# Kernel tuning notes

Hardware: AMD Instinct MI355X
Metric: run time of the kernel (lower is better)

The kernel has to match this reference:

```python
import jax, jax.numpy as jnp
import numpy as np

B, L, NF = 8, 4096, 256
NEG = jnp.float32(-1e30)
EPS = 1e-4  # scn BatchNormReLU default eps


def setup_inputs() -> dict:
    key = jax.random.key(0)
    ks = jax.random.split(key, 5)
    x = jax.random.normal(ks[0], (B, L, NF), dtype=jnp.float32)
    # ragged segment lengths -> padded mask
    lens = np.random.default_rng(0).integers(L // 2, L + 1, size=B)
    mask = jnp.asarray(np.arange(L)[None, :] < lens[:, None])  # [B, L] bool
    s = 1.0 / np.sqrt(NF)
    Wq = jax.random.normal(ks[1], (NF, NF), dtype=jnp.float32) * s
    Wk = jax.random.normal(ks[2], (NF, NF), dtype=jnp.float32) * s
    Wv = jax.random.normal(ks[3], (NF, NF), dtype=jnp.float32) * s
    Wt = jax.random.normal(ks[4], (NF, NF), dtype=jnp.float32) * s
    gamma = jnp.ones((NF,), dtype=jnp.float32)
    beta = jnp.zeros((NF,), dtype=jnp.float32)
    return {"x": x, "mask": mask, "Wq": Wq, "Wk": Wk, "Wv": Wv,
            "Wt": Wt, "gamma": gamma, "beta": beta}


def reference(x, mask, Wq, Wk, Wv, Wt, gamma, beta):
    m = mask.astype(x.dtype)[:, :, None]          # [B, L, 1] validity
    q = jnp.einsum('bld,de->ble', x, Wq)
    k = jnp.einsum('bld,de->ble', x, Wk)
    v = jnp.einsum('bld,de->ble', x, Wv)
    # per-segment full attention (unscaled QK^T, as in the original module)
    scores = jnp.einsum('bld,bmd->blm', q, k)     # [B, L, L]
    scores = jnp.where(mask[:, None, :], scores, NEG)
    p = jax.nn.softmax(scores, axis=-1)
    attn = jnp.einsum('blm,bmd->bld', p, v)
    t = jnp.einsum('bld,de->ble', attn, Wt)
    # BatchNormReLU over all valid points (masked batch stats per channel)
    n = jnp.sum(m)
    mean = jnp.sum(t * m, axis=(0, 1)) / n
    var = jnp.sum(jnp.square(t - mean) * m, axis=(0, 1)) / n
    y = gamma * (t - mean) * jax.lax.rsqrt(var + EPS) + beta
    y = jax.nn.relu(y)
    out = (x + y) * m                             # residual, zero padding
    return out
```

## Files before the change

### kernel.cpp

```cpp
#include <hip/hip_runtime.h>
#include <cmath>

typedef _Float16 f16;
typedef f16 f16x8 __attribute__((ext_vector_type(8)));
typedef f16 f16x4 __attribute__((ext_vector_type(4)));
typedef float f32x4 __attribute__((ext_vector_type(4)));

#define Ln 4096
#define Dn 256
#define NEGV (-1e30f)

#define B_QH   0ul
#define B_KH   (16ul << 20)
#define B_VT   (32ul << 20)
#define B_OP   (48ul << 20)
#define B_ML   (80ul << 20)
#define B_ATH  0ul
#define B_T    (16ul << 20)
#define B_LENS (81ul << 20)
#define B_SUMS (B_LENS + 128)
#define B_WQT  (B_LENS + 4096)
#define B_WKT  (B_WQT + (128ul<<10))
#define B_WVT  (B_WKT + (128ul<<10))
#define B_WTT  (B_WVT + (128ul<<10))

__device__ __forceinline__ void async_ld16(f16* lds, const f16* g) {
  __builtin_amdgcn_global_load_lds((const __attribute__((address_space(1))) unsigned int*)g,
                                   (__attribute__((address_space(3))) unsigned int*)lds, 16, 0, 0);
}

__global__ __launch_bounds__(256) void k_init(const int* __restrict__ mask, int* __restrict__ lens,
                                              float* __restrict__ sums) {
  const int b = blockIdx.x, tid = threadIdx.x;
  if (b == 0) { sums[tid] = 0.f; sums[256 + tid] = 0.f; }
  int cnt = 0;
  for (int l = tid; l < Ln; l += 256) cnt += (mask[b * Ln + l] != 0) ? 1 : 0;
  __shared__ int red[256];
  red[tid] = cnt;
  __syncthreads();
  for (int s = 128; s > 0; s >>= 1) {
    if (tid < s) red[tid] += red[tid + s];
    __syncthreads();
  }
  if (tid == 0) lens[b] = red[0];
}

__global__ __launch_bounds__(256) void k_cast_w(const float* __restrict__ W0, const float* __restrict__ W1,
                                                const float* __restrict__ W2, const float* __restrict__ W3,
                                                f16* __restrict__ T0, f16* __restrict__ T1,
                                                f16* __restrict__ T2, f16* __restrict__ T3) {
  const float* Ws[4] = {W0, W1, W2, W3};
  f16* Ts[4] = {T0, T1, T2, T3};
  const float* W = Ws[blockIdx.x];
  f16* T = Ts[blockIdx.x];
  const int k0 = blockIdx.y * 64, n0 = blockIdx.z * 64;
  const int tid = threadIdx.x;
  __shared__ float ld[64][65];
#pragma unroll
  for (int i = 0; i < 16; ++i) {
    int flat = i * 256 + tid;
    int r = flat >> 6, c = flat & 63;
    ld[r][c] = W[(size_t)(k0 + r) * Dn + n0 + c];
  }
  __syncthreads();
#pragma unroll
  for (int i = 0; i < 16; ++i) {
    int flat = i * 256 + tid;
    int r = flat >> 6, c = flat & 63;
    T[(size_t)(n0 + r) * Dn + k0 + c] = (f16)ld[c][r];
  }
}

__global__ __launch_bounds__(256) void k_qkv(const float* __restrict__ x, const f16* __restrict__ WqT,
                                             const f16* __restrict__ WkT, const f16* __restrict__ WvT,
                                             f16* __restrict__ Qh, f16* __restrict__ Kh,
                                             f16* __restrict__ Vt) {
  __shared__ f16 sA[64 * 256];
  __shared__ f16 vts[256 * 72];
  const int tid = threadIdx.x;
  const int lane = tid & 63;
  const int ln15 = lane & 15;
  const int quad = lane >> 4;
  const int wave = tid >> 6;
  const int wr = wave >> 1;
  const int wn = wave & 1;
  const size_t row0 = (size_t)blockIdx.x * 64;

  {
    const float* src = x + row0 * Dn;
#pragma unroll
    for (int i = 0; i < 8; ++i) {
      int flat = i * 256 + tid;
      int r = flat >> 5, p = flat & 31, g = p ^ (r & 7);
      float4 lo = *(const float4*)&src[r * Dn + g * 8];
      float4 hi = *(const float4*)&src[r * Dn + g * 8 + 4];
      f16x8 h = {(f16)lo.x, (f16)lo.y, (f16)lo.z, (f16)lo.w,
                 (f16)hi.x, (f16)hi.y, (f16)hi.z, (f16)hi.w};
      *(f16x8*)&sA[flat * 8] = h;
    }
  }
  __syncthreads();

  f16x8 af[2][8];
#pragma unroll
  for (int rg = 0; rg < 2; ++rg) {
    int r = wr * 32 + rg * 16 + ln15;
    int sw = r & 7;
#pragma unroll
    for (int c = 0; c < 8; ++c)
      af[rg][c] = *(const f16x8*)&sA[r * 256 + (((c * 4 + quad) ^ sw) << 3)];
  }

  const f16* Bm[3] = {WqT, WkT, WvT};
  for (int m = 0; m < 3; ++m) {
    const f16* B = Bm[m];
    f32x4 acc0[8], acc1[8];
#pragma unroll
    for (int nt = 0; nt < 8; ++nt) {
#pragma unroll
      for (int i = 0; i < 4; ++i) { acc0[nt][i] = 0.f; acc1[nt][i] = 0.f; }
    }
#pragma unroll
    for (int c = 0; c < 8; ++c) {
#pragma unroll
      for (int nt = 0; nt < 8; ++nt) {
        f16x8 bf = *(const f16x8*)&B[(size_t)(wn * 128 + nt * 16 + ln15) * 256 + c * 32 + quad * 8];
        acc0[nt] = __builtin_amdgcn_mfma_f32_16x16x32_f16(af[0][c], bf, acc0[nt], 0, 0, 0);
        acc1[nt] = __builtin_amdgcn_mfma_f32_16x16x32_f16(af[1][c], bf, acc1[nt], 0, 0, 0);
      }
    }
    if (m < 2) {
      f16* dst = (m == 0) ? Qh : Kh;
#pragma unroll
      for (int nt = 0; nt < 8; ++nt) {
        int col = wn * 128 + nt * 16 + ln15;
#pragma unroll
        for (int i = 0; i < 4; ++i) {
          dst[(row0 + wr * 32 + quad * 4 + i) * (size_t)Dn + col] = (f16)acc0[nt][i];
          dst[(row0 + wr * 32 + 16 + quad * 4 + i) * (size_t)Dn + col] = (f16)acc1[nt][i];
        }
      }
    } else {
#pragma unroll
      for (int nt = 0; nt < 8; ++nt) {
        int ch = wn * 128 + nt * 16 + ln15;
#pragma unroll
        for (int i = 0; i < 4; ++i) {
          vts[ch * 72 + wr * 32 + quad * 4 + i] = (f16)acc0[nt][i];
          vts[ch * 72 + wr * 32 + 16 + quad * 4 + i] = (f16)acc1[nt][i];
        }
      }
      __syncthreads();
      const int b = (int)(row0 >> 12);
      const int l0 = (int)(row0 & 4095);
      f16* vdst = Vt + (size_t)b * Dn * Ln + (size_t)tid * Ln + l0;
#pragma unroll
      for (int j = 0; j < 8; ++j)
        *(f16x8*)(vdst + 8 * j) = *(const f16x8*)&vts[tid * 72 + 8 * j];
    }
  }
}

__global__ __launch_bounds__(256, 3) void k_flash(const f16* __restrict__ Qh, const f16* __restrict__ Kh,
                                                  const f16* __restrict__ Vt, const int* __restrict__ lens,
                                                  f16* __restrict__ Op, float2* __restrict__ Ml) {
  const int b = blockIdx.z;
  const int s = blockIdx.y;
  const int len = lens[b];
  const int i0 = blockIdx.x * 64;
  if (i0 >= len) return;
  const int tid = threadIdx.x;
  const int lane = tid & 63;
  const int ln15 = lane & 15;
  const int quad = lane >> 4;
  const int w = tid >> 6;

  __shared__ f16 sK[32 * 256];
  __shared__ f16 sV[256 * 32];
  __shared__ f16 sP[4][16 * 40];

  const f16* Qb = Qh + (size_t)b * Ln * Dn;
  const f16* Kb = Kh + (size_t)b * Ln * Dn;
  const f16* Vb = Vt + (size_t)b * Dn * Ln;

  const int T = (len + 31) >> 5;
  const int h = T >> 1;
  const int t0 = s ? h : 0;
  const int t1 = s ? T : h;

  f16x8 qf[8];
  {
    const f16* qrow = Qb + (size_t)(i0 + w * 16 + ln15) * Dn + quad * 8;
#pragma unroll
    for (int c = 0; c < 8; ++c) qf[c] = *(const f16x8*)(qrow + c * 32);
  }

  f32x4 oAcc[16];
#pragma unroll
  for (int nf = 0; nf < 16; ++nf) { oAcc[nf][0] = 0.f; oAcc[nf][1] = 0.f; oAcc[nf][2] = 0.f; oAcc[nf][3] = 0.f; }
  float m_i[4], l_i[4];
#pragma unroll
  for (int i = 0; i < 4; ++i) { m_i[i] = -INFINITY; l_i[i] = 0.f; }

  for (int t = t0; t < t1; ++t) {
    const int j0 = t << 5;
    __syncthreads();
    {
      const f16* ksrc = Kb + (size_t)j0 * Dn;
#pragma unroll
      for (int i = 0; i < 4; ++i) {
        int flat = i * 256 + tid;
        int r = flat >> 5, p = flat & 31, g = p ^ (r & 7);
        async_ld16(&sK[(i * 256 + (tid & 192)) * 8], ksrc + r * Dn + g * 8);
      }
#pragma unroll
      for (int i = 0; i < 4; ++i) {
        int flat = i * 256 + tid;
        int r = flat >> 2, p = flat & 3, g = p ^ (r & 3);
        async_ld16(&sV[(i * 256 + (tid & 192)) * 8], Vb + (size_t)r * Ln + j0 + g * 8);
      }
    }
    __syncthreads();

    f32x4 sa0, sa1;
    sa0[0] = sa0[1] = sa0[2] = sa0[3] = 0.f;
    sa1[0] = sa1[1] = sa1[2] = sa1[3] = 0.f;
    const int swz = ln15 & 7;
#pragma unroll
    for (int c = 0; c < 8; ++c) {
      int gk = (((c * 4 + quad) ^ swz) << 3);
      f16x8 b0 = *(const f16x8*)&sK[ln15 * 256 + gk];
      f16x8 b1 = *(const f16x8*)&sK[(16 + ln15) * 256 + gk];
      sa0 = __builtin_amdgcn_mfma_f32_16x16x32_f16(qf[c], b0, sa0, 0, 0, 0);
      sa1 = __builtin_amdgcn_mfma_f32_16x16x32_f16(qf[c], b1, sa1, 0, 0, 0);
    }

    const bool iv0 = (j0 + ln15) >= len;
    const bool iv1 = (j0 + 16 + ln15) >= len;
    float alpha[4];
    bool need = false;
#pragma unroll
    for (int i = 0; i < 4; ++i) {
      float a0 = iv0 ? NEGV : sa0[i];
      float a1 = iv1 ? NEGV : sa1[i];
      float rm = fmaxf(a0, a1);
      rm = fmaxf(rm, __shfl_xor(rm, 1));
      rm = fmaxf(rm, __shfl_xor(rm, 2));
      rm = fmaxf(rm, __shfl_xor(rm, 4));
      rm = fmaxf(rm, __shfl_xor(rm, 8));
      float mo = m_i[i];
      float mn = fmaxf(mo, rm);
      float al = __expf(mo - mn);
      float p0 = __expf(a0 - mn);
      float p1 = __expf(a1 - mn);
      float rs = p0 + p1;
      rs += __shfl_xor(rs, 1);
      rs += __shfl_xor(rs, 2);
      rs += __shfl_xor(rs, 4);
      rs += __shfl_xor(rs, 8);
      l_i[i] = l_i[i] * al + rs;
      m_i[i] = mn;
      alpha[i] = al;
      need |= (al < 1.0f);
      sP[w][(quad * 4 + i) * 40 + ln15] = (f16)p0;
      sP[w][(quad * 4 + i) * 40 + 16 + ln15] = (f16)p1;
    }
    if (__any(need ? 1 : 0)) {
#pragma unroll
      for (int nf = 0; nf < 16; ++nf)
#pragma unroll
        for (int i = 0; i < 4; ++i) oAcc[nf][i] *= alpha[i];
    }

    f16x8 pa = *(const f16x8*)&sP[w][ln15 * 40 + quad * 8];
#pragma unroll
    for (int nf = 0; nf < 16; ++nf) {
      int ch = nf * 16 + ln15;
      f16x8 vb = *(const f16x8*)&sV[ch * 32 + ((quad ^ (ch & 3)) << 3)];
      oAcc[nf] = __builtin_amdgcn_mfma_f32_16x16x32_f16(pa, vb, oAcc[nf], 0, 0, 0);
    }
  }

  f16* Ob = Op + ((size_t)s * 8 + b) * Ln * Dn;
  float2* Mb = Ml + ((size_t)s * 8 + b) * Ln;
#pragma unroll
  for (int i = 0; i < 4; ++i) {
    int row = i0 + w * 16 + quad * 4 + i;
    if (row < len) {
      float inv = 1.f / l_i[i];
#pragma unroll
      for (int nf = 0; nf < 16; ++nf)
        Ob[(size_t)row * Dn + nf * 16 + ln15] = (f16)(oAcc[nf][i] * inv);
      if (ln15 == 0) Mb[row] = make_float2(m_i[i], l_i[i]);
    }
  }
}

__global__ __launch_bounds__(256) void k_combine(const f16* __restrict__ Op, const float2* __restrict__ Ml,
                                                 const int* __restrict__ lens, f16* __restrict__ ath) {
  const size_t idx = (size_t)blockIdx.x * 256 + threadIdx.x;
  const size_t rowg = idx >> 6;
  const int b = (int)(rowg >> 12);
  const int row = (int)(rowg & 4095);
  if (row >= lens[b]) return;
  const size_t SS = (size_t)8 * Ln * Dn;
  float2 ml0 = Ml[(size_t)b * Ln + row];
  float2 ml1 = Ml[(size_t)8 * Ln + (size_t)b * Ln + row];
  float ms = fmaxf(ml0.x, ml1.x);
  float w0 = __expf(ml0.x - ms) * ml0.y;
  float w1 = __expf(ml1.x - ms) * ml1.y;
  float inv = 1.f / (w0 + w1);
  w0 *= inv; w1 *= inv;
  const size_t off = rowg * Dn + (idx & 63) * 4;
  f16x4 p0 = *(const f16x4*)&Op[off];
  f16x4 p1 = *(const f16x4*)&Op[SS + off];
  f16x4 o;
#pragma unroll
  for (int j = 0; j < 4; ++j) o[j] = (f16)(w0 * (float)p0[j] + w1 * (float)p1[j]);
  *(f16x4*)&ath[off] = o;
}

__global__ __launch_bounds__(256) void k_t(const f16* __restrict__ ah, const f16* __restrict__ WtT,
                                           const int* __restrict__ mask, float* __restrict__ t,
                                           float* __restrict__ sums) {
  __shared__ f16 sA[64 * 256];
  __shared__ float sSum[256];
  __shared__ float sSq[256];
  const int tid = threadIdx.x;
  const int lane = tid & 63;
  const int ln15 = lane & 15;
  const int quad = lane >> 4;
  const int wave = tid >> 6;
  const int wr = wave >> 1;
  const int wn = wave & 1;
  const size_t row0 = (size_t)blockIdx.x * 64;
  sSum[tid] = 0.f;
  sSq[tid] = 0.f;
  {
    const f16* src = ah + row0 * Dn;
#pragma unroll
    for (int i = 0; i < 8; ++i) {
      int flat = i * 256 + tid;
      int r = flat >> 5, p = flat & 31, g = p ^ (r & 7);
      async_ld16(&sA[(i * 256 + (tid & 192)) * 8], src + r * 256 + g * 8);
    }
  }
  __syncthreads();
  f16x8 af[2][8];
#pragma unroll
  for (int rg = 0; rg < 2; ++rg) {
    int r = wr * 32 + rg * 16 + ln15;
    int sw = r & 7;
#pragma unroll
    for (int c = 0; c < 8; ++c)
      af[rg][c] = *(const f16x8*)&sA[r * 256 + (((c * 4 + quad) ^ sw) << 3)];
  }
  f32x4 acc0[8], acc1[8];
#pragma unroll
  for (int nt = 0; nt < 8; ++nt) {
#pragma unroll
    for (int i = 0; i < 4; ++i) { acc0[nt][i] = 0.f; acc1[nt][i] = 0.f; }
  }
#pragma unroll
  for (int c = 0; c < 8; ++c) {
#pragma unroll
    for (int nt = 0; nt < 8; ++nt) {
      f16x8 bf = *(const f16x8*)&WtT[(size_t)(wn * 128 + nt * 16 + ln15) * 256 + c * 32 + quad * 8];
      acc0[nt] = __builtin_amdgcn_mfma_f32_16x16x32_f16(af[0][c], bf, acc0[nt], 0, 0, 0);
      acc1[nt] = __builtin_amdgcn_mfma_f32_16x16x32_f16(af[1][c], bf, acc1[nt], 0, 0, 0);
    }
  }
  float msk0[4], msk1[4];
#pragma unroll
  for (int i = 0; i < 4; ++i) {
    size_t r = row0 + wr * 32 + quad * 4 + i;
    msk0[i] = (mask[r] != 0) ? 1.f : 0.f;
    msk1[i] = (mask[r + 16] != 0) ? 1.f : 0.f;
  }
#pragma unroll
  for (int nt = 0; nt < 8; ++nt) {
    int col = wn * 128 + nt * 16 + ln15;
    float ps = 0.f, pq = 0.f;
#pragma unroll
    for (int i = 0; i < 4; ++i) {
      float v0 = acc0[nt][i], v1 = acc1[nt][i];
      t[(row0 + wr * 32 + quad * 4 + i) * (size_t)Dn + col] = v0;
      t[(row0 + wr * 32 + 16 + quad * 4 + i) * (size_t)Dn + col] = v1;
      ps += v0 * msk0[i] + v1 * msk1[i];
      pq += v0 * v0 * msk0[i] + v1 * v1 * msk1[i];
    }
    ps += __shfl_xor(ps, 16); ps += __shfl_xor(ps, 32);
    pq += __shfl_xor(pq, 16); pq += __shfl_xor(pq, 32);
    if (quad == 0) {
      atomicAdd(&sSum[col], ps);
      atomicAdd(&sSq[col], pq);
    }
  }
  __syncthreads();
  atomicAdd(&sums[tid], sSum[tid]);
  atomicAdd(&sums[256 + tid], sSq[tid]);
}

__device__ __forceinline__ float bn_relu(float tv, int ch, float fn, const float* sums,
                                         const float* gamma, const float* beta) {
  float mean = sums[ch] / fn;
  float var = sums[256 + ch] / fn - mean * mean;
  float y = gamma[ch] * (tv - mean) * rsqrtf(var + 1e-4f) + beta[ch];
  return y > 0.f ? y : 0.f;
}

__global__ __launch_bounds__(256) void k_final(const float* __restrict__ x, const int* __restrict__ mask,
                                               const float* __restrict__ t, const float* __restrict__ gamma,
                                               const float* __restrict__ beta, const float* __restrict__ sums,
                                               const int* __restrict__ lens, float* __restrict__ out) {
  const size_t idx = (size_t)blockIdx.x * 256 + threadIdx.x;
  const size_t row = idx >> 6;
  const int c = (int)(idx & 63) * 4;
  float4 o;
  if (mask[row] == 0) {
    o = make_float4(0.f, 0.f, 0.f, 0.f);
  } else {
    int n = 0;
#pragma unroll
    for (int i = 0; i < 8; ++i) n += lens[i];
    const float fn = (float)n;
    float4 tv = *(const float4*)&t[row * Dn + c];
    float4 xv = *(const float4*)&x[row * Dn + c];
    o.x = xv.x + bn_relu(tv.x, c + 0, fn, sums, gamma, beta);
    o.y = xv.y + bn_relu(tv.y, c + 1, fn, sums, gamma, beta);
    o.z = xv.z + bn_relu(tv.z, c + 2, fn, sums, gamma, beta);
    o.w = xv.w + bn_relu(tv.w, c + 3, fn, sums, gamma, beta);
  }
  *(float4*)&out[idx * 4] = o;
}

extern "C" void kernel_launch(void* const* d_in, const int* in_sizes, int n_in,
                              void* d_out, int out_size, void* d_ws, size_t ws_size,
                              hipStream_t stream) {
  const float* x = (const float*)d_in[0];
  const int* mask = (const int*)d_in[1];
  const float* Wq = (const float*)d_in[2];
  const float* Wk = (const float*)d_in[3];
  const float* Wv = (const float*)d_in[4];
  const float* Wt = (const float*)d_in[5];
  const float* gamma = (const float*)d_in[6];
  const float* beta = (const float*)d_in[7];
  float* out = (float*)d_out;
  char* wsb = (char*)d_ws;

  f16* Qh = (f16*)(wsb + B_QH);
  f16* Kh = (f16*)(wsb + B_KH);
  f16* Vt = (f16*)(wsb + B_VT);
  f16* Op = (f16*)(wsb + B_OP);
  float2* Ml = (float2*)(wsb + B_ML);
  f16* ath = (f16*)(wsb + B_ATH);
  float* t = (float*)(wsb + B_T);
  int* lens = (int*)(wsb + B_LENS);
  float* sums = (float*)(wsb + B_SUMS);
  f16* WqT = (f16*)(wsb + B_WQT);
  f16* WkT = (f16*)(wsb + B_WKT);
  f16* WvT = (f16*)(wsb + B_WVT);
  f16* WtT = (f16*)(wsb + B_WTT);

  k_init<<<8, 256, 0, stream>>>(mask, lens, sums);
  k_cast_w<<<dim3(4, 4, 4), 256, 0, stream>>>(Wq, Wk, Wv, Wt, WqT, WkT, WvT, WtT);
  k_qkv<<<512, 256, 0, stream>>>(x, WqT, WkT, WvT, Qh, Kh, Vt);
  k_flash<<<dim3(64, 2, 8), 256, 0, stream>>>(Qh, Kh, Vt, lens, Op, Ml);
  k_combine<<<8192, 256, 0, stream>>>(Op, Ml, lens, ath);
  k_t<<<512, 256, 0, stream>>>(ath, WtT, mask, t, sums);
  k_final<<<8192, 256, 0, stream>>>(x, mask, t, gamma, beta, sums, lens, out);
}
```

Baseline: 463.2 us.

## Split flash attention three ways, fold combine into projection, MFMA row sums

The key range in the flash kernel is now split into three parts instead of two, giving more blocks to spread across the GPU. The separate combine kernel is removed: the output-projection kernel now reads the three partial outputs and their max/sum statistics, merges them with softmax weights while filling LDS, and then does the GEMM. The per-row softmax denominator is accumulated with an MFMA against a ones vector instead of shuffle reductions. In exchange it writes and reads a third partial output buffer, repeats the Q loads for each split, and replaces async LDS loads in the projection kernel with synchronous loads plus arithmetic.

After: 395.0 us. 1.17x faster.

```diff
diff --git a/kernel.cpp b/kernel.cpp
--- a/kernel.cpp
+++ b/kernel.cpp
@@ -14,10 +14,9 @@
 #define B_KH   (16ul << 20)
 #define B_VT   (32ul << 20)
 #define B_OP   (48ul << 20)
-#define B_ML   (80ul << 20)
-#define B_ATH  0ul
+#define B_ML   (96ul << 20)
 #define B_T    (16ul << 20)
-#define B_LENS (81ul << 20)
+#define B_LENS ((97ul << 20))
 #define B_SUMS (B_LENS + 128)
 #define B_WQT  (B_LENS + 4096)
 #define B_WKT  (B_WQT + (128ul<<10))
@@ -184,9 +183,8 @@
   const f16* Vb = Vt + (size_t)b * Dn * Ln;
 
   const int T = (len + 31) >> 5;
-  const int h = T >> 1;
-  const int t0 = s ? h : 0;
-  const int t1 = s ? T : h;
+  const int t0 = (s * T) / 3;
+  const int t1 = ((s + 1) * T) / 3;
 
   f16x8 qf[8];
   {
@@ -198,9 +196,13 @@
   f32x4 oAcc[16];
 #pragma unroll
   for (int nf = 0; nf < 16; ++nf) { oAcc[nf][0] = 0.f; oAcc[nf][1] = 0.f; oAcc[nf][2] = 0.f; oAcc[nf][3] = 0.f; }
-  float m_i[4], l_i[4];
-#pragma unroll
-  for (int i = 0; i < 4; ++i) { m_i[i] = -INFINITY; l_i[i] = 0.f; }
+  f32x4 lAcc;
+  lAcc[0] = lAcc[1] = lAcc[2] = lAcc[3] = 0.f;
+  float m_i[4];
+#pragma unroll
+  for (int i = 0; i < 4; ++i) m_i[i] = -INFINITY;
+  const f16x8 onesf = {(f16)1.f, (f16)1.f, (f16)1.f, (f16)1.f,
+                       (f16)1.f, (f16)1.f, (f16)1.f, (f16)1.f};
 
   for (int t = t0; t < t1; ++t) {
     const int j0 = t << 5;
@@ -253,12 +255,6 @@
       float al = __expf(mo - mn);
       float p0 = __expf(a0 - mn);
       float p1 = __expf(a1 - mn);
-      float rs = p0 + p1;
-      rs += __shfl_xor(rs, 1);
-      rs += __shfl_xor(rs, 2);
-      rs += __shfl_xor(rs, 4);
-      rs += __shfl_xor(rs, 8);
-      l_i[i] = l_i[i] * al + rs;
       m_i[i] = mn;
       alpha[i] = al;
       need |= (al < 1.0f);
@@ -270,9 +266,12 @@
       for (int nf = 0; nf < 16; ++nf)
 #pragma unroll
         for (int i = 0; i < 4; ++i) oAcc[nf][i] *= alpha[i];
+#pragma unroll
+      for (int i = 0; i < 4; ++i) lAcc[i] *= alpha[i];
     }
 
     f16x8 pa = *(const f16x8*)&sP[w][ln15 * 40 + quad * 8];
+    lAcc = __builtin_amdgcn_mfma_f32_16x16x32_f16(pa, onesf, lAcc, 0, 0, 0);
 #pragma unroll
     for (int nf = 0; nf < 16; ++nf) {
       int ch = nf * 16 + ln15;
@@ -281,49 +280,27 @@
     }
   }
 
-  f16* Ob = Op + ((size_t)s * 8 + b) * Ln * Dn;
+  f16* Ob = Op + (size_t)s * (8ul * Ln * Dn) + (size_t)b * Ln * Dn;
   float2* Mb = Ml + ((size_t)s * 8 + b) * Ln;
 #pragma unroll
   for (int i = 0; i < 4; ++i) {
     int row = i0 + w * 16 + quad * 4 + i;
     if (row < len) {
-      float inv = 1.f / l_i[i];
+      float inv = 1.f / lAcc[i];
 #pragma unroll
       for (int nf = 0; nf < 16; ++nf)
         Ob[(size_t)row * Dn + nf * 16 + ln15] = (f16)(oAcc[nf][i] * inv);
-      if (ln15 == 0) Mb[row] = make_float2(m_i[i], l_i[i]);
-    }
-  }
-}
-
-__global__ __launch_bounds__(256) void k_combine(const f16* __restrict__ Op, const float2* __restrict__ Ml,
-                                                 const int* __restrict__ lens, f16* __restrict__ ath) {
-  const size_t idx = (size_t)blockIdx.x * 256 + threadIdx.x;
-  const size_t rowg = idx >> 6;
-  const int b = (int)(rowg >> 12);
-  const int row = (int)(rowg & 4095);
-  if (row >= lens[b]) return;
-  const size_t SS = (size_t)8 * Ln * Dn;
-  float2 ml0 = Ml[(size_t)b * Ln + row];
-  float2 ml1 = Ml[(size_t)8 * Ln + (size_t)b * Ln + row];
-  float ms = fmaxf(ml0.x, ml1.x);
-  float w0 = __expf(ml0.x - ms) * ml0.y;
-  float w1 = __expf(ml1.x - ms) * ml1.y;
-  float inv = 1.f / (w0 + w1);
-  w0 *= inv; w1 *= inv;
-  const size_t off = rowg * Dn + (idx & 63) * 4;
-  f16x4 p0 = *(const f16x4*)&Op[off];
-  f16x4 p1 = *(const f16x4*)&Op[SS + off];
-  f16x4 o;
-#pragma unroll
-  for (int j = 0; j < 4; ++j) o[j] = (f16)(w0 * (float)p0[j] + w1 * (float)p1[j]);
-  *(f16x4*)&ath[off] = o;
-}
-
-__global__ __launch_bounds__(256) void k_t(const f16* __restrict__ ah, const f16* __restrict__ WtT,
-                                           const int* __restrict__ mask, float* __restrict__ t,
+      if (ln15 == 0) Mb[row] = make_float2(m_i[i], lAcc[i]);
+    }
+  }
+}
+
+__global__ __launch_bounds__(256) void k_t(const f16* __restrict__ Op, const float2* __restrict__ Ml,
+                                           const f16* __restrict__ WtT, const int* __restrict__ mask,
+                                           const int* __restrict__ lens, float* __restrict__ t,
                                            float* __restrict__ sums) {
   __shared__ f16 sA[64 * 256];
+  __shared__ float sW[3][64];
   __shared__ float sSum[256];
   __shared__ float sSq[256];
   const int tid = threadIdx.x;
@@ -334,16 +311,42 @@
   const int wr = wave >> 1;
   const int wn = wave & 1;
   const size_t row0 = (size_t)blockIdx.x * 64;
+  const int b = (int)(row0 >> 12);
+  const int r0loc = (int)(row0 & 4095);
+  const size_t SS = 8ul * Ln * Dn;
   sSum[tid] = 0.f;
   sSq[tid] = 0.f;
-  {
-    const f16* src = ah + row0 * Dn;
-#pragma unroll
-    for (int i = 0; i < 8; ++i) {
-      int flat = i * 256 + tid;
-      int r = flat >> 5, p = flat & 31, g = p ^ (r & 7);
-      async_ld16(&sA[(i * 256 + (tid & 192)) * 8], src + r * 256 + g * 8);
-    }
+  if (tid < 64) {
+    int rl = r0loc + tid;
+    float w0 = 0.f, w1 = 0.f, w2 = 0.f;
+    if (rl < lens[b]) {
+      float2 m0 = Ml[(size_t)(0 * 8 + b) * Ln + rl];
+      float2 m1 = Ml[(size_t)(1 * 8 + b) * Ln + rl];
+      float2 m2 = Ml[(size_t)(2 * 8 + b) * Ln + rl];
+      float ms = fmaxf(m0.x, fmaxf(m1.x, m2.x));
+      w0 = __expf(m0.x - ms) * m0.y;
+      w1 = __expf(m1.x - ms) * m1.y;
+      w2 = __expf(m2.x - ms) * m2.y;
+      float inv = 1.f / (w0 + w1 + w2);
+      w0 *= inv; w1 *= inv; w2 *= inv;
+    }
+    sW[0][tid] = w0; sW[1][tid] = w1; sW[2][tid] = w2;
+  }
+  __syncthreads();
+#pragma unroll
+  for (int i = 0; i < 8; ++i) {
+    int flat = i * 256 + tid;
+    int r = flat >> 5, p = flat & 31, g = p ^ (r & 7);
+    size_t off = (row0 + r) * (size_t)Dn + g * 8;
+    f16x8 p0 = *(const f16x8*)&Op[off];
+    f16x8 p1 = *(const f16x8*)&Op[SS + off];
+    f16x8 p2 = *(const f16x8*)&Op[2 * SS + off];
+    float w0 = sW[0][r], w1 = sW[1][r], w2 = sW[2][r];
+    f16x8 h;
+#pragma unroll
+    for (int j = 0; j < 8; ++j)
+      h[j] = (f16)(w0 * (float)p0[j] + w1 * (float)p1[j] + w2 * (float)p2[j]);
+    *(f16x8*)&sA[flat * 8] = h;
   }
   __syncthreads();
   f16x8 af[2][8];
@@ -453,7 +456,6 @@
   f16* Vt = (f16*)(wsb + B_VT);
   f16* Op = (f16*)(wsb + B_OP);
   float2* Ml = (float2*)(wsb + B_ML);
-  f16* ath = (f16*)(wsb + B_ATH);
   float* t = (float*)(wsb + B_T);
   int* lens = (int*)(wsb + B_LENS);
   float* sums = (float*)(wsb + B_SUMS);
@@ -465,8 +467,7 @@
   k_init<<<8, 256, 0, stream>>>(mask, lens, sums);
   k_cast_w<<<dim3(4, 4, 4), 256, 0, stream>>>(Wq, Wk, Wv, Wt, WqT, WkT, WvT, WtT);
   k_qkv<<<512, 256, 0, stream>>>(x, WqT, WkT, WvT, Qh, Kh, Vt);
-  k_flash<<<dim3(64, 2, 8), 256, 0, stream>>>(Qh, Kh, Vt, lens, Op, Ml);
-  k_combine<<<8192, 256, 0, stream>>>(Op, Ml, lens, ath);
-  k_t<<<512, 256, 0, stream>>>(ath, WtT, mask, t, sums);
+  k_flash<<<dim3(64, 3, 8), 256, 0, stream>>>(Qh, Kh, Vt, lens, Op, Ml);
+  k_t<<<512, 256, 0, stream>>>(Op, Ml, WtT, mask, lens, t, sums);
   k_final<<<8192, 256, 0, stream>>>(x, mask, t, gamma, beta, sums, lens, out);
 }
```
